# Optimization experiments

Hardware: AMD Instinct MI355X
Metric: run time of the kernel (lower is better)

The kernel has to match this reference:

```python
import jax, jax.numpy as jnp
import numpy as np

B, N, F_IN, F_HID, F_OUT = 64, 1024, 64, 128, 64

def setup_inputs() -> dict:
    key = jax.random.key(0)
    ks = jax.random.split(key, 6)
    x = jax.random.normal(ks[0], (B, N, F_IN), dtype=jnp.float32)
    adj = jax.random.uniform(ks[1], (B, N, N), dtype=jnp.float32)
    mask = jax.random.randint(ks[2], (B, N), 0, 2).astype(bool)
    W1 = jax.random.normal(ks[3], (F_IN, F_HID), dtype=jnp.float32) * (1.0 / np.sqrt(F_IN))
    b1 = jnp.zeros((F_HID,), dtype=jnp.float32)
    W2 = jax.random.normal(ks[4], (F_HID, F_OUT), dtype=jnp.float32) * (1.0 / np.sqrt(F_HID))
    b2 = jnp.zeros((F_OUT,), dtype=jnp.float32)
    eps = jnp.zeros((1,), dtype=jnp.float32)
    return {"x": x, "adj": adj, "mask": mask, "W1": W1, "b1": b1, "W2": W2, "b2": b2, "eps": eps}

def reference(x, adj, mask, W1, b1, W2, b2, eps):
    # neighbor aggregation: out[b,i,f] = sum_j adj[b,i,j] * x[b,j,f]
    agg = jnp.einsum('bij,bjf->bif', adj, x)
    # add_loop=True: (1 + eps) * x + aggregated neighbors
    h = (1.0 + eps[0]) * x + agg
    # 2-layer GIN MLP applied per node (only valid nodes contribute in the
    # torch version via gather/scatter; invalid positions are zeroed)
    h = jax.nn.relu(h @ W1 + b1) @ W2 + b2
    return jnp.where(mask[..., None], h, jnp.zeros((), dtype=h.dtype))
```

## Files before the change

kernel.cpp:

```cpp
#include <hip/hip_runtime.h>


#define N_     1024
#define FIN    64
#define FHID   128
#define FOUT   64
#define HS_LD  68
#define H1_LD  132
#define CH     64
#define NCHUNK 16
#define KSPC   4
#define FROW   9
#define AUNITS 18
#define ABUFU  1152
#define ADJ_BYTES 18432
#define XSU    512

typedef __attribute__((ext_vector_type(16))) float f32x16;
typedef __attribute__((ext_vector_type(8)))  short s16x8;
typedef __attribute__((ext_vector_type(4)))  short s16x4;

__device__ inline short f2bf(float f) {
    union { float f; unsigned int u; } v; v.f = f;
    unsigned int r = v.u + 0x7fffu + ((v.u >> 16) & 1u);
    return (short)(r >> 16);
}

__global__ __launch_bounds__(256, 3) void gin_main(
    const float* __restrict__ x, const float* __restrict__ adj,
    const int* __restrict__ mask, const float* __restrict__ W1,
    const float* __restrict__ b1, const float* __restrict__ W2,
    const float* __restrict__ b2, const float* __restrict__ epsp,
    float* __restrict__ out)
{
    __shared__ __align__(16) char region_raw[34816];
    __shared__ float hs[64 * HS_LD];

    auto   asf  = reinterpret_cast<s16x8 (*)[64][FROW]>(region_raw);
    s16x4* asf4 = reinterpret_cast<s16x4*>(region_raw);
    s16x8* xsb  = reinterpret_cast<s16x8*>(region_raw + ADJ_BYTES);
    float* h1s  = reinterpret_cast<float*>(region_raw);

    const int t    = threadIdx.x;
    const int lane = t & 63;
    const int w    = t >> 6;
    const int b    = blockIdx.x >> 4;
    const int i0   = (blockIdx.x & 15) * 64;

    const float* xb   = x   + (size_t)b * N_ * FIN;
    const float* adjb = adj + (size_t)b * N_ * N_ + (size_t)i0 * N_;

    const int l31  = lane & 31;
    const int half = lane >> 5;
    const int mrow = (w & 1) * 32;
    const int ncol = (w >> 1) * 32;
    const int ngq  = (w >> 1);

    const int rq16 = t >> 4;
    const int cl16 = t & 15;
    const float* adjA = adjb + (size_t)rq16 * N_ + cl16 * 4;

    const int gx = t >> 5;
    const int mx = t & 31;
    const float* xrow0 = xb + (size_t)(gx * 8) * FIN + 2 * mx;
    const int slotA = gx * 64 + mx;

    const int sbase = ngq * 16 + (l31 >> 1) + ((l31 & 1) << 5);

    f32x16 acc;
    #pragma unroll
    for (int r = 0; r < 16; ++r) acc[r] = 0.f;

    float4 areg[2][4];
    float2 xregf[2][8];

    #define ISSUE_A(p, c_) { _Pragma("unroll") for (int q = 0; q < 4; ++q) \
        areg[p][q] = *reinterpret_cast<const float4*>(adjA + (size_t)q * 16 * N_ + (size_t)(c_) * CH); }
    #define ISSUE_X(p, c_) { _Pragma("unroll") for (int k = 0; k < 8; ++k) \
        xregf[p][k] = *reinterpret_cast<const float2*>(xrow0 + (size_t)((c_) * CH + k) * FIN); }
    #define STAGE_A(o, p) { _Pragma("unroll") for (int q = 0; q < 4; ++q) { \
        const float4 u = areg[p][q]; s16x4 fr; \
        fr[0] = f2bf(u.x); fr[1] = f2bf(u.y); fr[2] = f2bf(u.z); fr[3] = f2bf(u.w); \
        asf4[(o) * ABUFU + (q * 16 + rq16) * AUNITS + cl16] = fr; } }
    #define STAGE_X(o, p) { s16x8 frA, frB; \
        _Pragma("unroll") for (int k = 0; k < 8; ++k) { \
            frA[k] = f2bf(xregf[p][k].x); frB[k] = f2bf(xregf[p][k].y); } \
        xsb[(o) * XSU + slotA] = frA; xsb[(o) * XSU + slotA + 32] = frB; }

    ISSUE_A(0, 0); ISSUE_A(1, 1);
    ISSUE_X(0, 0); ISSUE_X(1, 1);
    STAGE_A(0, 0);
    STAGE_X(0, 0);
    asm volatile("s_waitcnt lgkmcnt(0)" ::: "memory");
    __builtin_amdgcn_s_barrier();

    #pragma unroll
    for (int c = 0; c < NCHUNK; ++c) {
        if (c + 2 < NCHUNK) {
            ISSUE_A(c & 1, c + 2);
            ISSUE_X(c & 1, c + 2);
        }
        #pragma unroll
        for (int s = 0; s < KSPC; ++s) {
            const s16x8 a  = asf[c & 1][mrow + l31][2 * s + half];
            const s16x8 bb = xsb[(c & 1) * XSU + (s * 2 + half) * 64 + sbase];
            acc = __builtin_amdgcn_mfma_f32_32x32x16_bf16(a, bb, acc, 0, 0, 0);
        }
        if (c + 1 < NCHUNK) {
            STAGE_A((c + 1) & 1, (c + 1) & 1);
            STAGE_X((c + 1) & 1, (c + 1) & 1);
            asm volatile("s_waitcnt lgkmcnt(0)" ::: "memory");
            __builtin_amdgcn_s_barrier();
        }
    }

    {
        const float se = 1.0f + epsp[0];
        const int col = ncol + l31;
        #pragma unroll
        for (int reg = 0; reg < 16; ++reg) {
            const int row = mrow + (reg & 3) + 8 * (reg >> 2) + 4 * half;
            const float xv = xb[(size_t)(i0 + row) * FIN + col];
            hs[row * HS_LD + col] = acc[reg] + se * xv;
        }
    }
    __syncthreads();

    {
        const int k4 = (t & 31) * 4;
        const int rb = (t >> 5) * 8;
        float4 hacc[8];
        const float4 b1v = *reinterpret_cast<const float4*>(b1 + k4);
        #pragma unroll
        for (int r = 0; r < 8; ++r) hacc[r] = b1v;

        #pragma unroll 4
        for (int j = 0; j < FIN; ++j) {
            const float4 w1v = *reinterpret_cast<const float4*>(W1 + j * FHID + k4);
            #pragma unroll
            for (int r = 0; r < 8; ++r) {
                const float hv = hs[(rb + r) * HS_LD + j];
                hacc[r].x += hv * w1v.x; hacc[r].y += hv * w1v.y;
                hacc[r].z += hv * w1v.z; hacc[r].w += hv * w1v.w;
            }
        }
        #pragma unroll
        for (int r = 0; r < 8; ++r) {
            float4 v;
            v.x = fmaxf(hacc[r].x, 0.f); v.y = fmaxf(hacc[r].y, 0.f);
            v.z = fmaxf(hacc[r].z, 0.f); v.w = fmaxf(hacc[r].w, 0.f);
            *reinterpret_cast<float4*>(&h1s[(rb + r) * H1_LD + k4]) = v;
        }
    }
    __syncthreads();

    {
        const int fi = (t & 15) * 4;
        const int ri = (t >> 4) * 4;
        float4 oacc[4];
        const float4 b2v = *reinterpret_cast<const float4*>(b2 + fi);
        #pragma unroll
        for (int ii = 0; ii < 4; ++ii) oacc[ii] = b2v;

        #pragma unroll 4
        for (int j = 0; j < FHID; ++j) {
            const float4 w2v = *reinterpret_cast<const float4*>(W2 + j * FOUT + fi);
            #pragma unroll
            for (int ii = 0; ii < 4; ++ii) {
                const float hv = h1s[(ri + ii) * H1_LD + j];
                oacc[ii].x += hv * w2v.x; oacc[ii].y += hv * w2v.y;
                oacc[ii].z += hv * w2v.z; oacc[ii].w += hv * w2v.w;
            }
        }
        #pragma unroll
        for (int ii = 0; ii < 4; ++ii) {
            const int gi = i0 + ri + ii;
            const int m  = mask[b * N_ + gi];
            float4 o = oacc[ii];
            if (!m) o = make_float4(0.f, 0.f, 0.f, 0.f);
            *reinterpret_cast<float4*>(out + ((size_t)b * N_ + gi) * FOUT + fi) = o;
        }
    }
}

extern "C" void kernel_launch(void* const* d_in, const int* in_sizes, int n_in,
                              void* d_out, int out_size, void* d_ws, size_t ws_size,
                              hipStream_t stream) {
    const float* x    = (const float*)d_in[0];
    const float* adj  = (const float*)d_in[1];
    const int*   mask = (const int*)  d_in[2];
    const float* W1   = (const float*)d_in[3];
    const float* b1   = (const float*)d_in[4];
    const float* W2   = (const float*)d_in[5];
    const float* b2   = (const float*)d_in[6];
    const float* eps  = (const float*)d_in[7];
    float* out = (float*)d_out;
    (void)d_ws; (void)ws_size;

    gin_main<<<dim3(64 * 16), dim3(256), 0, stream>>>(x, adj, mask, W1, b1, W2, b2, eps, out);
}
```

Before: 424.0 us.

## Run both GIN MLP layers on bf16 MFMA with prepacked weight fragments

Both MLP layers now run as bf16 32x32x16 MFMA instead of scalar fp32 FMA loops. A small pre-kernel converts W1 and W2 into bf16 MFMA fragments in workspace. The hidden activations are stored as swizzled bf16 inside the shared adjacency region, which removes the separate hs buffer, cuts LDS use and raises the occupancy hint to 4. The x prefetch is also reduced to a single buffer issued one chunk ahead, which lowers register pressure. Rounding the hidden activations to bf16 costs some precision, and the extra launch adds a small fixed cost.

```diff
diff --git a/kernel.cpp b/kernel.cpp
--- a/kernel.cpp
+++ b/kernel.cpp
@@ -5,16 +5,15 @@
 #define FIN    64
 #define FHID   128
 #define FOUT   64
-#define HS_LD  68
-#define H1_LD  132
 #define CH     64
 #define NCHUNK 16
 #define KSPC   4
-#define FROW   9
 #define AUNITS 18
 #define ABUFU  1152
 #define ADJ_BYTES 18432
 #define XSU    512
+#define H1OFF  8192
+#define REGION 34816
 
 typedef __attribute__((ext_vector_type(16))) float f32x16;
 typedef __attribute__((ext_vector_type(8)))  short s16x8;
@@ -26,20 +25,36 @@
     return (short)(r >> 16);
 }
 
-__global__ __launch_bounds__(256, 3) void gin_main(
+__global__ __launch_bounds__(256) void wpack(const float* __restrict__ W1,
+                                             const float* __restrict__ W2,
+                                             s16x8* __restrict__ wf)
+{
+    const int u = blockIdx.x * 256 + threadIdx.x;
+    s16x8 fr;
+    if (u < 1024) {
+        const int ks2 = u >> 7, col = u & 127;
+        #pragma unroll
+        for (int k = 0; k < 8; ++k) fr[k] = f2bf(W1[(ks2 * 8 + k) * FHID + col]);
+    } else {
+        const int v = u - 1024;
+        const int ks2 = v >> 6, col = v & 63;
+        #pragma unroll
+        for (int k = 0; k < 8; ++k) fr[k] = f2bf(W2[(ks2 * 8 + k) * FOUT + col]);
+    }
+    wf[u] = fr;
+}
+
+__global__ __launch_bounds__(256, 4) void gin_main(
     const float* __restrict__ x, const float* __restrict__ adj,
-    const int* __restrict__ mask, const float* __restrict__ W1,
-    const float* __restrict__ b1, const float* __restrict__ W2,
+    const int* __restrict__ mask, const float* __restrict__ b1,
     const float* __restrict__ b2, const float* __restrict__ epsp,
-    float* __restrict__ out)
+    const s16x8* __restrict__ wf, float* __restrict__ out)
 {
-    __shared__ __align__(16) char region_raw[34816];
-    __shared__ float hs[64 * HS_LD];
-
-    auto   asf  = reinterpret_cast<s16x8 (*)[64][FROW]>(region_raw);
+    __shared__ __align__(16) char region_raw[REGION];
+
+    auto   asf  = reinterpret_cast<s16x8 (*)[64][AUNITS / 2]>(region_raw);
     s16x4* asf4 = reinterpret_cast<s16x4*>(region_raw);
     s16x8* xsb  = reinterpret_cast<s16x8*>(region_raw + ADJ_BYTES);
-    float* h1s  = reinterpret_cast<float*>(region_raw);
 
     const int t    = threadIdx.x;
     const int lane = t & 63;
@@ -53,8 +68,8 @@
     const int l31  = lane & 31;
     const int half = lane >> 5;
     const int mrow = (w & 1) * 32;
-    const int ncol = (w >> 1) * 32;
     const int ngq  = (w >> 1);
+    const int ncol = ngq * 32;
 
     const int rq16 = t >> 4;
     const int cl16 = t & 15;
@@ -72,34 +87,32 @@
     for (int r = 0; r < 16; ++r) acc[r] = 0.f;
 
     float4 areg[2][4];
-    float2 xregf[2][8];
+    float2 xregf[8];
 
     #define ISSUE_A(p, c_) { _Pragma("unroll") for (int q = 0; q < 4; ++q) \
         areg[p][q] = *reinterpret_cast<const float4*>(adjA + (size_t)q * 16 * N_ + (size_t)(c_) * CH); }
-    #define ISSUE_X(p, c_) { _Pragma("unroll") for (int k = 0; k < 8; ++k) \
-        xregf[p][k] = *reinterpret_cast<const float2*>(xrow0 + (size_t)((c_) * CH + k) * FIN); }
+    #define ISSUE_X(c_) { _Pragma("unroll") for (int k = 0; k < 8; ++k) \
+        xregf[k] = *reinterpret_cast<const float2*>(xrow0 + (size_t)((c_) * CH + k) * FIN); }
     #define STAGE_A(o, p) { _Pragma("unroll") for (int q = 0; q < 4; ++q) { \
         const float4 u = areg[p][q]; s16x4 fr; \
         fr[0] = f2bf(u.x); fr[1] = f2bf(u.y); fr[2] = f2bf(u.z); fr[3] = f2bf(u.w); \
         asf4[(o) * ABUFU + (q * 16 + rq16) * AUNITS + cl16] = fr; } }
-    #define STAGE_X(o, p) { s16x8 frA, frB; \
+    #define STAGE_X(o) { s16x8 frA, frB; \
         _Pragma("unroll") for (int k = 0; k < 8; ++k) { \
-            frA[k] = f2bf(xregf[p][k].x); frB[k] = f2bf(xregf[p][k].y); } \
+            frA[k] = f2bf(xregf[k].x); frB[k] = f2bf(xregf[k].y); } \
         xsb[(o) * XSU + slotA] = frA; xsb[(o) * XSU + slotA + 32] = frB; }
 
     ISSUE_A(0, 0); ISSUE_A(1, 1);
-    ISSUE_X(0, 0); ISSUE_X(1, 1);
+    ISSUE_X(0);
     STAGE_A(0, 0);
-    STAGE_X(0, 0);
+    STAGE_X(0);
     asm volatile("s_waitcnt lgkmcnt(0)" ::: "memory");
     __builtin_amdgcn_s_barrier();
 
     #pragma unroll
     for (int c = 0; c < NCHUNK; ++c) {
-        if (c + 2 < NCHUNK) {
-            ISSUE_A(c & 1, c + 2);
-            ISSUE_X(c & 1, c + 2);
-        }
+        if (c + 2 < NCHUNK) ISSUE_A(c & 1, c + 2);
+        if (c + 1 < NCHUNK) ISSUE_X(c + 1);
         #pragma unroll
         for (int s = 0; s < KSPC; ++s) {
             const s16x8 a  = asf[c & 1][mrow + l31][2 * s + half];
@@ -108,77 +121,82 @@
         }
         if (c + 1 < NCHUNK) {
             STAGE_A((c + 1) & 1, (c + 1) & 1);
-            STAGE_X((c + 1) & 1, (c + 1) & 1);
+            STAGE_X((c + 1) & 1);
             asm volatile("s_waitcnt lgkmcnt(0)" ::: "memory");
             __builtin_amdgcn_s_barrier();
         }
     }
+    __syncthreads();
 
     {
         const float se = 1.0f + epsp[0];
         const int col = ncol + l31;
         #pragma unroll
-        for (int reg = 0; reg < 16; ++reg) {
-            const int row = mrow + (reg & 3) + 8 * (reg >> 2) + 4 * half;
+        for (int r = 0; r < 16; ++r) {
+            const int row = mrow + (r & 3) + 8 * (r >> 2) + 4 * half;
             const float xv = xb[(size_t)(i0 + row) * FIN + col];
-            hs[row * HS_LD + col] = acc[reg] + se * xv;
+            const float hv = acc[r] + se * xv;
+            const int byte = (row * 128 + col * 2) ^ ((row & 7) << 4);
+            *reinterpret_cast<unsigned short*>(region_raw + byte) = (unsigned short)f2bf(hv);
         }
     }
     __syncthreads();
 
     {
-        const int k4 = (t & 31) * 4;
-        const int rb = (t >> 5) * 8;
-        float4 hacc[8];
-        const float4 b1v = *reinterpret_cast<const float4*>(b1 + k4);
-        #pragma unroll
-        for (int r = 0; r < 8; ++r) hacc[r] = b1v;
-
-        #pragma unroll 4
-        for (int j = 0; j < FIN; ++j) {
-            const float4 w1v = *reinterpret_cast<const float4*>(W1 + j * FHID + k4);
-            #pragma unroll
-            for (int r = 0; r < 8; ++r) {
-                const float hv = hs[(rb + r) * HS_LD + j];
-                hacc[r].x += hv * w1v.x; hacc[r].y += hv * w1v.y;
-                hacc[r].z += hv * w1v.z; hacc[r].w += hv * w1v.w;
-            }
-        }
-        #pragma unroll
-        for (int r = 0; r < 8; ++r) {
-            float4 v;
-            v.x = fmaxf(hacc[r].x, 0.f); v.y = fmaxf(hacc[r].y, 0.f);
-            v.z = fmaxf(hacc[r].z, 0.f); v.w = fmaxf(hacc[r].w, 0.f);
-            *reinterpret_cast<float4*>(&h1s[(rb + r) * H1_LD + k4]) = v;
+        const int mB  = w & 1;
+        const int nB0 = w >> 1;
+        f32x16 acc0, acc1;
+        const float bv0 = b1[nB0 * 32 + l31];
+        const float bv1 = b1[(nB0 + 2) * 32 + l31];
+        #pragma unroll
+        for (int r = 0; r < 16; ++r) { acc0[r] = bv0; acc1[r] = bv1; }
+        const int hrow = mB * 32 + l31;
+        #pragma unroll
+        for (int ks = 0; ks < 4; ++ks) {
+            const int hb = (hrow * 128 + ks * 32 + half * 16) ^ ((hrow & 7) << 4);
+            const s16x8 a   = *reinterpret_cast<const s16x8*>(region_raw + hb);
+            const s16x8 w1a = wf[(ks * 2 + half) * 128 + nB0 * 32 + l31];
+            const s16x8 w1b = wf[(ks * 2 + half) * 128 + (nB0 + 2) * 32 + l31];
+            acc0 = __builtin_amdgcn_mfma_f32_32x32x16_bf16(a, w1a, acc0, 0, 0, 0);
+            acc1 = __builtin_amdgcn_mfma_f32_32x32x16_bf16(a, w1b, acc1, 0, 0, 0);
+        }
+        __syncthreads();
+        #pragma unroll
+        for (int r = 0; r < 16; ++r) {
+            const int row = mB * 32 + (r & 3) + 8 * (r >> 2) + 4 * half;
+            const int c0 = nB0 * 32 + l31, c1 = (nB0 + 2) * 32 + l31;
+            const int y0 = H1OFF + ((row * 256 + c0 * 2) ^ ((row & 7) << 4));
+            const int y1 = H1OFF + ((row * 256 + c1 * 2) ^ ((row & 7) << 4));
+            *reinterpret_cast<unsigned short*>(region_raw + y0) =
+                (unsigned short)f2bf(fmaxf(acc0[r], 0.f));
+            *reinterpret_cast<unsigned short*>(region_raw + y1) =
+                (unsigned short)f2bf(fmaxf(acc1[r], 0.f));
         }
     }
     __syncthreads();
 
     {
-        const int fi = (t & 15) * 4;
-        const int ri = (t >> 4) * 4;
-        float4 oacc[4];
-        const float4 b2v = *reinterpret_cast<const float4*>(b2 + fi);
-        #pragma unroll
-        for (int ii = 0; ii < 4; ++ii) oacc[ii] = b2v;
-
-        #pragma unroll 4
-        for (int j = 0; j < FHID; ++j) {
-            const float4 w2v = *reinterpret_cast<const float4*>(W2 + j * FOUT + fi);
-            #pragma unroll
-            for (int ii = 0; ii < 4; ++ii) {
-                const float hv = h1s[(ri + ii) * H1_LD + j];
-                oacc[ii].x += hv * w2v.x; oacc[ii].y += hv * w2v.y;
-                oacc[ii].z += hv * w2v.z; oacc[ii].w += hv * w2v.w;
-            }
-        }
-        #pragma unroll
-        for (int ii = 0; ii < 4; ++ii) {
-            const int gi = i0 + ri + ii;
-            const int m  = mask[b * N_ + gi];
-            float4 o = oacc[ii];
-            if (!m) o = make_float4(0.f, 0.f, 0.f, 0.f);
-            *reinterpret_cast<float4*>(out + ((size_t)b * N_ + gi) * FOUT + fi) = o;
+        const int mo = w & 1;
+        const int no = w >> 1;
+        f32x16 accC;
+        const float bv = b2[no * 32 + l31];
+        #pragma unroll
+        for (int r = 0; r < 16; ++r) accC[r] = bv;
+        const int arow = mo * 32 + l31;
+        #pragma unroll
+        for (int ks = 0; ks < 8; ++ks) {
+            const int hb = H1OFF + ((arow * 256 + ks * 32 + half * 16) ^ ((arow & 7) << 4));
+            const s16x8 a  = *reinterpret_cast<const s16x8*>(region_raw + hb);
+            const s16x8 wb = wf[1024 + (ks * 2 + half) * 64 + no * 32 + l31];
+            accC = __builtin_amdgcn_mfma_f32_32x32x16_bf16(a, wb, accC, 0, 0, 0);
+        }
+        const int col = no * 32 + l31;
+        #pragma unroll
+        for (int r = 0; r < 16; ++r) {
+            const int row = mo * 32 + (r & 3) + 8 * (r >> 2) + 4 * half;
+            const int gi = i0 + row;
+            const float v = mask[b * N_ + gi] ? accC[r] : 0.f;
+            out[((size_t)b * N_ + gi) * FOUT + col] = v;
         }
     }
 }
@@ -195,7 +213,8 @@
     const float* b2   = (const float*)d_in[6];
     const float* eps  = (const float*)d_in[7];
     float* out = (float*)d_out;
-    (void)d_ws; (void)ws_size;
-
-    gin_main<<<dim3(64 * 16), dim3(256), 0, stream>>>(x, adj, mask, W1, b1, W2, b2, eps, out);
-}
+    s16x8* wfrag = (s16x8*)d_ws;
+
+    wpack<<<dim3(8), dim3(256), 0, stream>>>(W1, W2, wfrag);
+    gin_main<<<dim3(64 * 16), dim3(256), 0, stream>>>(x, adj, mask, b1, b2, eps, wfrag, out);
+}
```

Result: faster. 398.5 us (-6.0%).
